# Kernel optimization log

Hardware: AMD Instinct MI355X
Metric: run time of the kernel (lower is better)

Reference implementation:

```python
import jax, jax.numpy as jnp
import numpy as np

B, S, H = 4, 4096, 1024
E, K, DE, DS = 8, 2, 128, 512  # n_routed_experts, top_k, routed hidden, shared hidden


def setup_inputs() -> dict:
    key = jax.random.key(0)
    ks = jax.random.split(key, 10)
    sc = 0.02
    return {
        "x": jax.random.normal(ks[0], (B, S, H), dtype=jnp.float32),
        "Wg": jax.random.normal(ks[1], (E, H), dtype=jnp.float32) * sc,
        "W1": jax.random.normal(ks[2], (E, DE, H), dtype=jnp.float32) * sc,
        "b1": jnp.zeros((E, DE), dtype=jnp.float32),
        "W2": jax.random.normal(ks[3], (E, H, DE), dtype=jnp.float32) * sc,
        "b2": jnp.zeros((E, H), dtype=jnp.float32),
        "Ws1": jax.random.normal(ks[4], (DS, H), dtype=jnp.float32) * sc,
        "bs1": jnp.zeros((DS,), dtype=jnp.float32),
        "Ws2": jax.random.normal(ks[5], (H, DS), dtype=jnp.float32) * sc,
        "bs2": jnp.zeros((H,), dtype=jnp.float32),
    }


def reference(x, Wg, W1, b1, W2, b2, Ws1, bs1, Ws2, bs2):
    # FFNMoE forward, eval mode (dropout = identity, aux loss inactive).
    xf = x.reshape(-1, H)  # [T, H]
    # --- MOEGate: softmax scoring + top-k + normalized weights ---
    logits = xf @ Wg.T                         # [T, E]
    scores = jax.nn.softmax(logits, axis=-1)
    topk_w, topk_idx = jax.lax.top_k(scores, K)  # [T, K]
    topk_w = topk_w / (jnp.sum(topk_w, axis=-1, keepdims=True) + 1e-20)
    # Dense per-(token, expert) combine weight (topk indices are distinct).
    w = jnp.sum(jax.nn.one_hot(topk_idx, E, dtype=xf.dtype) * topk_w[..., None], axis=1)  # [T, E]
    # --- Routed experts: fc1 -> relu -> fc2, weighted scatter-combine ---
    h1 = jax.nn.relu(jnp.einsum('th,efh->tef', xf, W1) + b1)       # [T, E, DE]
    y = jnp.einsum('tef,ehf,te->th', h1, W2, w) + w @ b2           # [T, H]
    # --- Shared expert ---
    sh = jax.nn.relu(xf @ Ws1.T + bs1) @ Ws2.T + bs2               # [T, H]
    return (y + sh).reshape(x.shape)
```

## Files before the change

### kernel.cpp

```cpp
#include <hip/hip_runtime.h>
#include <cstdint>

#define TTOK 16384
#define HD   1024
#define NE   8
#define NDE  128
#define NDS  512
#define NC1  1536
#define KC2  1536
#define NPAIR 28
#define MAXT  96
#define PREPB 3080
#define GATEB 1024
#define NH    768

typedef float  f32x4  __attribute__((ext_vector_type(4)));
typedef __bf16 bf16x8 __attribute__((ext_vector_type(8)));

__device__ __forceinline__ unsigned short f2bf(float f) {
  unsigned int u = __float_as_uint(f);
  u += 0x7fffu + ((u >> 16) & 1u);
  return (unsigned short)(u >> 16);
}

__device__ __forceinline__ void gl2lds16(const void* gp, void* lp) {
  void* g0 = const_cast<void*>(gp);
  __builtin_amdgcn_global_load_lds((__attribute__((address_space(1))) void*)g0,
                                   (__attribute__((address_space(3))) void*)lp,
                                   16, 0, 0);
}

__device__ __forceinline__ void barx() {
  asm volatile("" ::: "memory");
  __builtin_amdgcn_s_barrier();
  asm volatile("" ::: "memory");
}

template<int Q>
__device__ __forceinline__ void phase_reads(const unsigned short* Ab, const unsigned short* Bb,
                                            int bs, int a0, int b0,
                                            bf16x8 (&av)[4][2], bf16x8 (&bv)[2][2]) {
  constexpr int MH = Q >> 1, NHF = Q & 1;
  if constexpr (NHF == 0) {
#pragma unroll
    for (int m = 0; m < 4; ++m) {
      const int ao = a0 + (MH * 4 + m) * 1024;
      av[m][0] = *(const bf16x8*)(Ab + bs + ao);
      av[m][1] = *(const bf16x8*)(Ab + bs + (ao ^ 32));
    }
  }
#pragma unroll
  for (int n = 0; n < 2; ++n) {
    const int bo = b0 + (NHF * 2 + n) * 1024;
    bv[n][0] = *(const bf16x8*)(Bb + bs + bo);
    bv[n][1] = *(const bf16x8*)(Bb + bs + (bo ^ 32));
  }
}

template<int Q>
__device__ __forceinline__ void phase_mfma(bf16x8 (&av)[4][2], bf16x8 (&bv)[2][2],
                                           f32x4 (&acc)[8][4]) {
  constexpr int MH = Q >> 1, NHF = Q & 1;
  __builtin_amdgcn_s_setprio(1);
#pragma unroll
  for (int ks = 0; ks < 2; ++ks)
#pragma unroll
    for (int m = 0; m < 4; ++m)
#pragma unroll
      for (int n = 0; n < 2; ++n)
        acc[MH * 4 + m][NHF * 2 + n] = __builtin_amdgcn_mfma_f32_16x16x32_bf16(
            av[m][ks], bv[n][ks], acc[MH * 4 + m][NHF * 2 + n], 0, 0, 0);
  __builtin_amdgcn_s_setprio(0);
}

#define PH(Q, BH, STG, VMW) do {                                    \
    phase_reads<Q>(AsB, BsB, (BH) * 16384, a0, b0, av, bv);         \
    STG;                                                            \
    VMW;                                                            \
    barx();                                                         \
    asm volatile("s_waitcnt lgkmcnt(0)" ::: "memory");              \
    __builtin_amdgcn_sched_barrier(0);                              \
    phase_mfma<Q>(av, bv, acc);                                     \
    barx();                                                         \
  } while (0)

__global__ __launch_bounds__(256) void prep_gate(
    const float* __restrict__ x, const float* __restrict__ Wg,
    const float* __restrict__ W1, const float* __restrict__ Ws1,
    const float* __restrict__ W2, const float* __restrict__ Ws2,
    const float* __restrict__ b1, const float* __restrict__ bs1,
    unsigned short* __restrict__ W1cat, unsigned short* __restrict__ W2cat,
    float* __restrict__ bias1, unsigned short* __restrict__ xbf,
    float2* __restrict__ wpair, int* __restrict__ pid) {
  if (blockIdx.x < PREPB) {
    const int total = NC1 * HD + HD * KC2 + NC1;
    for (int idx = blockIdx.x * 256 + threadIdx.x; idx < total; idx += PREPB * 256) {
      if (idx < NC1 * HD) {
        int r = idx >> 10, k = idx & 1023;
        float v = (r < 1024) ? W1[idx] : Ws1[(size_t)(r - 1024) * HD + k];
        W1cat[idx] = f2bf(v);
      } else if (idx < NC1 * HD + HD * KC2) {
        int i2 = idx - NC1 * HD;
        int h = i2 / KC2;
        int j = i2 - h * KC2;
        float v = (j < 1024) ? W2[(size_t)((j >> 7) * HD + h) * NDE + (j & 127)]
                             : Ws2[(size_t)h * NDS + (j - 1024)];
        W2cat[i2] = f2bf(v);
      } else {
        int r = idx - (NC1 * HD + HD * KC2);
        bias1[r] = (r < 1024) ? b1[r] : bs1[r - 1024];
      }
    }
    return;
  }
  __shared__ float part[16 * 8 * 64];
  __shared__ float lgs[128];

  const int tid  = threadIdx.x;
  const int lane = tid & 63;
  const int wv   = tid >> 6;
  const int g    = blockIdx.x - PREPB;
  const int tokb = g * 16 + wv * 4;

  const float* xr = x + (size_t)tokb * HD + lane * 16;
  float4 xv[4][4];
#pragma unroll
  for (int t = 0; t < 4; ++t)
#pragma unroll
    for (int c = 0; c < 4; ++c)
      xv[t][c] = ((const float4*)(xr + (size_t)t * HD))[c];

#pragma unroll
  for (int t = 0; t < 4; ++t) {
    unsigned short* xo = xbf + (size_t)(tokb + t) * HD + lane * 16;
    union { unsigned short us[8]; uint4 v; } pk;
    pk.us[0] = f2bf(xv[t][0].x); pk.us[1] = f2bf(xv[t][0].y);
    pk.us[2] = f2bf(xv[t][0].z); pk.us[3] = f2bf(xv[t][0].w);
    pk.us[4] = f2bf(xv[t][1].x); pk.us[5] = f2bf(xv[t][1].y);
    pk.us[6] = f2bf(xv[t][1].z); pk.us[7] = f2bf(xv[t][1].w);
    ((uint4*)xo)[0] = pk.v;
    pk.us[0] = f2bf(xv[t][2].x); pk.us[1] = f2bf(xv[t][2].y);
    pk.us[2] = f2bf(xv[t][2].z); pk.us[3] = f2bf(xv[t][2].w);
    pk.us[4] = f2bf(xv[t][3].x); pk.us[5] = f2bf(xv[t][3].y);
    pk.us[6] = f2bf(xv[t][3].z); pk.us[7] = f2bf(xv[t][3].w);
    ((uint4*)xo)[1] = pk.v;
  }

  float p[4][8];
#pragma unroll
  for (int t = 0; t < 4; ++t)
#pragma unroll
    for (int e = 0; e < 8; ++e) p[t][e] = 0.f;
#pragma unroll
  for (int e = 0; e < 8; ++e) {
    const float4* wr = (const float4*)(Wg + (size_t)e * HD + lane * 16);
    float4 w0 = wr[0], w1 = wr[1], w2 = wr[2], w3 = wr[3];
#pragma unroll
    for (int t = 0; t < 4; ++t) {
      p[t][e] = w0.x * xv[t][0].x + w0.y * xv[t][0].y + w0.z * xv[t][0].z + w0.w * xv[t][0].w +
                w1.x * xv[t][1].x + w1.y * xv[t][1].y + w1.z * xv[t][1].z + w1.w * xv[t][1].w +
                w2.x * xv[t][2].x + w2.y * xv[t][2].y + w2.z * xv[t][2].z + w2.w * xv[t][2].w +
                w3.x * xv[t][3].x + w3.y * xv[t][3].y + w3.z * xv[t][3].z + w3.w * xv[t][3].w;
    }
  }
#pragma unroll
  for (int t = 0; t < 4; ++t)
#pragma unroll
    for (int e = 0; e < 8; ++e) {
      int j = (wv * 4 + t) * 8 + e;
      part[j * 64 + ((lane + 4 * j) & 63)] = p[t][e];
    }
  __syncthreads();

  if (tid < 128) {
    float s = 0.f;
#pragma unroll
    for (int m = 0; m < 16; ++m) {
      int kk = (4 * m + 4 * tid) & 63;
      float4 v = *(const float4*)&part[tid * 64 + kk];
      s += v.x + v.y + v.z + v.w;
    }
    lgs[tid] = s;
  }
  __syncthreads();

  if (tid < 16) {
    float lg[8];
#pragma unroll
    for (int e = 0; e < 8; ++e) lg[e] = lgs[tid * 8 + e];
    int i1 = 0; float m1 = lg[0];
#pragma unroll
    for (int e = 1; e < 8; ++e) { if (lg[e] > m1) { m1 = lg[e]; i1 = e; } }
    int i2 = -1; float m2 = -3.4e38f;
#pragma unroll
    for (int e = 0; e < 8; ++e) { if (e != i1 && lg[e] > m2) { m2 = lg[e]; i2 = e; } }
    float Z = 0.f;
#pragma unroll
    for (int e = 0; e < 8; ++e) Z += expf(lg[e] - m1);
    float s1 = 1.f / Z;
    float s2 = expf(m2 - m1) / Z;
    float dn = s1 + s2 + 1e-20f;
    float w1 = s1 / dn, w2 = s2 / dn;
    int ef, es; float wf, wsx;
    if (i1 < i2) { ef = i1; es = i2; wf = w1; wsx = w2; }
    else         { ef = i2; es = i1; wf = w2; wsx = w1; }
    int pq = ef * 7 - (ef * (ef - 1)) / 2 + (es - ef - 1);
    int t = g * 16 + tid;
    wpair[t] = make_float2(wf, wsx);
    pid[t] = pq;
  }
}

__global__ __launch_bounds__(256) void route_scan(const int* __restrict__ pid,
                                                  int* __restrict__ perm,
                                                  int4* __restrict__ tiletab,
                                                  int* __restrict__ ntct) {
  __shared__ int hist[256 * 29];
  __shared__ int totals[NPAIR];
  __shared__ int spre[256];
  const int p   = blockIdx.x;
  const int tid = threadIdx.x;
#pragma unroll
  for (int q = 0; q < 29; ++q) hist[tid * 29 + q] = 0;
  __syncthreads();
  for (int k = 0; k < 64; ++k) {
    int q = pid[tid + (k << 8)];
    hist[tid * 29 + q]++;
  }
  __syncthreads();
  if (tid < NPAIR) {
    int s = 0;
    for (int i = 0; i < 256; ++i) s += hist[i * 29 + tid];
    totals[tid] = s;
  }
  __syncthreads();
  const int mycnt = hist[tid * 29 + p];
  spre[tid] = mycnt;
  __syncthreads();
  for (int d = 1; d < 256; d <<= 1) {
    int add = (tid >= d) ? spre[tid - d] : 0;
    __syncthreads();
    spre[tid] += add;
    __syncthreads();
  }
  int estart = 0, tstart = 0;
  for (int q = 0; q < p; ++q) { estart += totals[q]; tstart += (totals[q] + 255) >> 8; }
  const int cp = totals[p];
  const int nt = (cp + 255) >> 8;
  if (p == NPAIR - 1 && tid == 0) ntct[0] = tstart + nt;
  for (int k = tid; k < nt; k += 256) {
    int4 e;
    e.x = p;
    e.y = estart + (k << 8);
    e.z = min(256, cp - (k << 8));
    e.w = (tstart + k) << 8;
    tiletab[tstart + k] = e;
  }
  int wr = estart + spre[tid] - mycnt;
  for (int k = 0; k < 64; ++k) {
    int t = tid + (k << 8);
    if (pid[t] == p) perm[wr++] = t;
  }
}

__global__ __launch_bounds__(512, 2) void moe_fc1(
    const unsigned short* __restrict__ xbf, const unsigned short* __restrict__ W1cat,
    const int* __restrict__ perm, const float2* __restrict__ wpair,
    const float* __restrict__ bias1, const int4* __restrict__ tiletab,
    const int* __restrict__ ntct, unsigned short* __restrict__ Hbuf) {
  const int L   = blockIdx.x;
  const int xcd = L & 7;
  const int s   = L >> 3;
  const int mg  = s / 3;
  const int nn  = s - mg * 3;
  const int mt  = xcd + (mg << 3);
  if (mt >= ntct[0]) return;
  const int4 tt = tiletab[mt];
  const int eoff = tt.y, valid = tt.z, hbase = tt.w;
  int ef = 0, rem = tt.x;
  while (rem >= 7 - ef) { rem -= 7 - ef; ef++; }
  const int es = ef + 1 + rem;

  __shared__ __align__(16) unsigned short As[2 * 16384];
  __shared__ __align__(16) unsigned short Bs[2 * 16384];

  const int tid  = threadIdx.x;
  const int lane = tid & 63;
  const int wv   = tid >> 6;
  const int wm   = wv >> 2;
  const int wn   = wv & 3;
  const int r16  = lane & 15;
  const int quad = lane >> 4;

  const unsigned short* gAp[2][2];
  const unsigned short* gBp[2][2];
  int lAo[2][2], lBo[2][2];
#pragma unroll
  for (int h = 0; h < 2; ++h)
#pragma unroll
    for (int jj = 0; jj < 2; ++jj) {
      const int id = jj * 512 + tid;
      const int rp = id >> 3, cc = id & 7;
      const int rowA = h * 64 + ((rp & 64) << 1) + (rp & 63);
      const int tok  = perm[eoff + min(rowA, valid - 1)];
      gAp[h][jj] = xbf + (size_t)tok * HD + ((cc ^ (rowA & 7)) << 3);
      lAo[h][jj] = rowA * 64 + cc * 8;
      const int rowB = h * 128 + rp;
      const int brow = (nn == 0) ? (((h == 0) ? ef : es) * 128 + rp)
                                 : 1024 + (nn - 1) * 256 + rowB;
      gBp[h][jj] = W1cat + (size_t)brow * HD + ((cc ^ (rowB & 7)) << 3);
      lBo[h][jj] = rowB * 64 + cc * 8;
    }

  unsigned short* AsB = As;
  unsigned short* BsB = Bs;

  const int swz = (quad ^ (r16 & 7)) << 3;
  const int a0 = (wm * 128 + r16) * 64 + swz;
  const int b0 = (wn * 64 + r16) * 64 + swz;

  f32x4 acc[8][4];
#pragma unroll
  for (int i = 0; i < 8; ++i)
#pragma unroll
    for (int j = 0; j < 4; ++j) acc[i][j] = (f32x4){0.f, 0.f, 0.f, 0.f};
  bf16x8 av[4][2], bv[2][2];

#define STG_A1K(t, h) do { const int b_ = (((t) & 1) << 14); const int o_ = ((t) << 6); \
    gl2lds16(gAp[h][0] + o_, AsB + b_ + lAo[h][0]);                                     \
    gl2lds16(gAp[h][1] + o_, AsB + b_ + lAo[h][1]); } while (0)
#define STG_B1K(t, h) do { const int b_ = (((t) & 1) << 14); const int o_ = ((t) << 6); \
    gl2lds16(gBp[h][0] + o_, BsB + b_ + lBo[h][0]);                                     \
    gl2lds16(gBp[h][1] + o_, BsB + b_ + lBo[h][1]); } while (0)

  STG_A1K(0, 0); STG_A1K(0, 1);
  STG_B1K(0, 0); STG_B1K(0, 1);
  STG_A1K(1, 0); STG_A1K(1, 1);
  asm volatile("s_waitcnt vmcnt(4)" ::: "memory");
  barx();

#define FC1_ITER(it, LASTF) do {                                                   \
    const int O1 = 2 * (it) + 1, E2 = 2 * (it) + 2, O2 = 2 * (it) + 3;             \
    PH(0, 0, STG_B1K(O1, 0), (void)0);                                             \
    PH(1, 0, STG_B1K(O1, 1), (void)0);                                             \
    PH(2, 0, { if (!(LASTF)) STG_A1K(E2, 0); }, (void)0);                          \
    PH(3, 0, { if (!(LASTF)) STG_A1K(E2, 1); },                                    \
        { if (LASTF) asm volatile("s_waitcnt vmcnt(0)" ::: "memory");              \
          else       asm volatile("s_waitcnt vmcnt(4)" ::: "memory"); });          \
    PH(0, 1, { if (!(LASTF)) STG_B1K(E2, 0); }, (void)0);                          \
    PH(1, 1, { if (!(LASTF)) STG_B1K(E2, 1); }, (void)0);                          \
    PH(2, 1, { if (!(LASTF)) STG_A1K(O2, 0); }, (void)0);                          \
    PH(3, 1, { if (!(LASTF)) STG_A1K(O2, 1); },                                    \
        { if (LASTF) asm volatile("s_waitcnt vmcnt(0)" ::: "memory");              \
          else       asm volatile("s_waitcnt vmcnt(4)" ::: "memory"); });          \
  } while (0)

#pragma unroll 1
  for (int it = 0; it < 7; ++it) FC1_ITER(it, 0);
  FC1_ITER(7, 1);

  __syncthreads();
  float2* wl = (float2*)As;
  if (tid < 256) {
    const int tokc = perm[eoff + min(tid, valid - 1)];
    wl[tid] = wpair[tokc];
  }
  __syncthreads();
  float bz[4];
  const int colb = wn * 64 + r16;
#pragma unroll
  for (int n2 = 0; n2 < 4; ++n2) {
    const int col = colb + n2 * 16;
    const int bidx = (nn == 0) ? ((col < 128) ? ef * 128 + col : es * 128 + (col - 128))
                               : 1024 + (nn - 1) * 256 + col;
    bz[n2] = bias1[bidx];
  }
#pragma unroll
  for (int m2 = 0; m2 < 8; ++m2) {
#pragma unroll
    for (int r = 0; r < 4; ++r) {
      const int lrow = wm * 128 + m2 * 16 + quad * 4 + r;
      const float2 w = wl[lrow];
      const float sc = (nn == 0) ? ((wn < 2) ? w.x : w.y) : 1.0f;
      unsigned short* hp = Hbuf + (size_t)(hbase + lrow) * NH + nn * 256 + colb;
#pragma unroll
      for (int n2 = 0; n2 < 4; ++n2) {
        const float v = fmaxf(acc[m2][n2][r] + bz[n2], 0.f) * sc;
        hp[n2 * 16] = f2bf(v);
      }
    }
  }
#undef FC1_ITER
#undef STG_A1K
#undef STG_B1K
}

__device__ __forceinline__ int koB2(int t, int ef, int es) {
  return (t < 2) ? ef * 128 + (t << 6)
       : (t < 4) ? es * 128 + ((t - 2) << 6)
                 : 1024 + ((t - 4) << 6);
}

__global__ __launch_bounds__(512, 2) void moe_fc2(
    const unsigned short* __restrict__ Hbuf, const unsigned short* __restrict__ W2cat,
    const int* __restrict__ perm, const float2* __restrict__ wpair,
    const float* __restrict__ b2, const float* __restrict__ bs2,
    const int4* __restrict__ tiletab, const int* __restrict__ ntct,
    float* __restrict__ out) {
  const int L   = blockIdx.x;
  const int xcd = L & 7;
  const int s   = L >> 3;
  const int mg  = s >> 2;
  const int nn  = s & 3;
  const int mt  = xcd + (mg << 3);
  if (mt >= ntct[0]) return;
  const int4 tt = tiletab[mt];
  const int eoff = tt.y, valid = tt.z, hbase = tt.w;
  int ef = 0, rem = tt.x;
  while (rem >= 7 - ef) { rem -= 7 - ef; ef++; }
  const int es = ef + 1 + rem;
  const int tileN = nn << 8;

  __shared__ __align__(16) unsigned short As[2 * 16384];
  __shared__ __align__(16) unsigned short Bs[2 * 16384];

  const int tid  = threadIdx.x;
  const int lane = tid & 63;
  const int wv   = tid >> 6;
  const int wm   = wv >> 2;
  const int wn   = wv & 3;
  const int r16  = lane & 15;
  const int quad = lane >> 4;

  const unsigned short* gAp[2][2];
  const unsigned short* gBp[2][2];
  int lAo[2][2], lBo[2][2];
#pragma unroll
  for (int h = 0; h < 2; ++h)
#pragma unroll
    for (int jj = 0; jj < 2; ++jj) {
      const int id = jj * 512 + tid;
      const int rp = id >> 3, cc = id & 7;
      const int rowA = h * 64 + ((rp & 64) << 1) + (rp & 63);
      gAp[h][jj] = Hbuf + (size_t)(hbase + rowA) * NH + ((cc ^ (rowA & 7)) << 3);
      lAo[h][jj] = rowA * 64 + cc * 8;
      const int rowB = h * 128 + rp;
      gBp[h][jj] = W2cat + (size_t)(tileN + rowB) * KC2 + ((cc ^ (rowB & 7)) << 3);
      lBo[h][jj] = rowB * 64 + cc * 8;
    }

  unsigned short* AsB = As;
  unsigned short* BsB = Bs;

  const int swz = (quad ^ (r16 & 7)) << 3;
  const int a0 = (wm * 128 + r16) * 64 + swz;
  const int b0 = (wn * 64 + r16) * 64 + swz;

  f32x4 acc[8][4];
#pragma unroll
  for (int i = 0; i < 8; ++i)
#pragma unroll
    for (int j = 0; j < 4; ++j) acc[i][j] = (f32x4){0.f, 0.f, 0.f, 0.f};
  bf16x8 av[4][2], bv[2][2];

#define STG_A2K(t, h) do { const int b_ = (((t) & 1) << 14); const int o_ = ((t) << 6); \
    gl2lds16(gAp[h][0] + o_, AsB + b_ + lAo[h][0]);                                     \
    gl2lds16(gAp[h][1] + o_, AsB + b_ + lAo[h][1]); } while (0)
#define STG_B2K(t, h) do { const int b_ = (((t) & 1) << 14); const int o_ = koB2((t), ef, es); \
    gl2lds16(gBp[h][0] + o_, BsB + b_ + lBo[h][0]);                                     \
    gl2lds16(gBp[h][1] + o_, BsB + b_ + lBo[h][1]); } while (0)

  STG_A2K(0, 0); STG_A2K(0, 1);
  STG_B2K(0, 0); STG_B2K(0, 1);
  STG_A2K(1, 0); STG_A2K(1, 1);
  asm volatile("s_waitcnt vmcnt(4)" ::: "memory");
  barx();

#define FC2_ITER(it, LASTF) do {                                                   \
    const int O1 = 2 * (it) + 1, E2 = 2 * (it) + 2, O2 = 2 * (it) + 3;             \
    PH(0, 0, STG_B2K(O1, 0), (void)0);                                             \
    PH(1, 0, STG_B2K(O1, 1), (void)0);                                             \
    PH(2, 0, { if (!(LASTF)) STG_A2K(E2, 0); }, (void)0);                          \
    PH(3, 0, { if (!(LASTF)) STG_A2K(E2, 1); },                                    \
        { if (LASTF) asm volatile("s_waitcnt vmcnt(0)" ::: "memory");              \
          else       asm volatile("s_waitcnt vmcnt(4)" ::: "memory"); });          \
    PH(0, 1, { if (!(LASTF)) STG_B2K(E2, 0); }, (void)0);                          \
    PH(1, 1, { if (!(LASTF)) STG_B2K(E2, 1); }, (void)0);                          \
    PH(2, 1, { if (!(LASTF)) STG_A2K(O2, 0); }, (void)0);                          \
    PH(3, 1, { if (!(LASTF)) STG_A2K(O2, 1); },                                    \
        { if (LASTF) asm volatile("s_waitcnt vmcnt(0)" ::: "memory");              \
          else       asm volatile("s_waitcnt vmcnt(4)" ::: "memory"); });          \
  } while (0)

#pragma unroll 1
  for (int it = 0; it < 5; ++it) FC2_ITER(it, 0);
  FC2_ITER(5, 1);

  __syncthreads();
  float2* wl2 = (float2*)As;
  int* tokl   = (int*)Bs;
  if (tid < 256) {
    const int tokc = perm[eoff + min(tid, valid - 1)];
    tokl[tid] = (tid < valid) ? tokc : -1;
    wl2[tid] = wpair[tokc];
  }
  __syncthreads();
  float bsc[4], b2a[4], b2b[4];
  const int colb = tileN + wn * 64 + r16;
#pragma unroll
  for (int n2 = 0; n2 < 4; ++n2) {
    const int col = colb + n2 * 16;
    bsc[n2] = bs2[col];
    b2a[n2] = b2[(size_t)ef * HD + col];
    b2b[n2] = b2[(size_t)es * HD + col];
  }
#pragma unroll
  for (int m2 = 0; m2 < 8; ++m2) {
#pragma unroll
    for (int r = 0; r < 4; ++r) {
      const int lrow = wm * 128 + m2 * 16 + quad * 4 + r;
      const int tok = tokl[lrow];
      if (tok < 0) continue;
      const float2 w = wl2[lrow];
      float* op = out + (size_t)tok * HD + colb;
#pragma unroll
      for (int n2 = 0; n2 < 4; ++n2)
        op[n2 * 16] = acc[m2][n2][r] + bsc[n2] + w.x * b2a[n2] + w.y * b2b[n2];
    }
  }
#undef FC2_ITER
#undef STG_A2K
#undef STG_B2K
}

extern "C" void kernel_launch(void* const* d_in, const int* in_sizes, int n_in,
                              void* d_out, int out_size, void* d_ws, size_t ws_size,
                              hipStream_t stream) {
  const float* x   = (const float*)d_in[0];
  const float* Wg  = (const float*)d_in[1];
  const float* W1  = (const float*)d_in[2];
  const float* b1  = (const float*)d_in[3];
  const float* W2  = (const float*)d_in[4];
  const float* b2  = (const float*)d_in[5];
  const float* Ws1 = (const float*)d_in[6];
  const float* bs1 = (const float*)d_in[7];
  const float* Ws2 = (const float*)d_in[8];
  const float* bs2 = (const float*)d_in[9];

  char* ws = (char*)d_ws;
  size_t off = 0;
  unsigned short* xbf   = (unsigned short*)(ws + off); off += (size_t)TTOK * HD * 2;
  unsigned short* Hbuf  = (unsigned short*)(ws + off); off += (size_t)MAXT * 256 * NH * 2;
  unsigned short* W1cat = (unsigned short*)(ws + off); off += (size_t)NC1 * HD * 2;
  unsigned short* W2cat = (unsigned short*)(ws + off); off += (size_t)HD * KC2 * 2;
  float* bias1          = (float*)(ws + off);          off += (size_t)NC1 * 4;
  float2* wpair         = (float2*)(ws + off);         off += (size_t)TTOK * 8;
  int* pid              = (int*)(ws + off);            off += (size_t)TTOK * 4;
  int* perm             = (int*)(ws + off);            off += (size_t)TTOK * 4;
  int4* tiletab         = (int4*)(ws + off);           off += (size_t)MAXT * 16;
  int* ntct             = (int*)(ws + off);            off += 16;

  prep_gate<<<PREPB + GATEB, 256, 0, stream>>>(x, Wg, W1, Ws1, W2, Ws2, b1, bs1,
                                               W1cat, W2cat, bias1, xbf, wpair, pid);
  route_scan<<<NPAIR, 256, 0, stream>>>(pid, perm, tiletab, ntct);
  moe_fc1<<<8 * 12 * 3, 512, 0, stream>>>(xbf, W1cat, perm, wpair, bias1, tiletab, ntct, Hbuf);
  moe_fc2<<<8 * 12 * 4, 512, 0, stream>>>(Hbuf, W2cat, perm, wpair, b2, bs2, tiletab, ntct,
                                          (float*)d_out);
}
```

Before: 294.7 us.

## Reschedule fc1 staging pipeline and replace fc2 with smaller-tile single-buffered GEMM

The fc1 kernel's global-to-LDS staging schedule is reshuffled: A half-tiles are issued earlier, vmcnt waits are tightened to 2, partial lgkmcnt waits are added, and the sched_barrier is dropped. The fc2 kernel is replaced by a simpler 128x128-tile, 256-thread kernel with a single LDS buffer and 16 blocks per routing tile. This adds occupancy and parallelism for fc2 but gives up its double-buffered phased pipeline, so load latency is exposed at each of the two syncthreads per K step. Fewer accumulators per thread also lowers register pressure.

```diff
diff --git a/kernel.cpp b/kernel.cpp
--- a/kernel.cpp
+++ b/kernel.cpp
@@ -58,8 +58,8 @@
 }
 
 template<int Q>
-__device__ __forceinline__ void phase_mfma(bf16x8 (&av)[4][2], bf16x8 (&bv)[2][2],
-                                           f32x4 (&acc)[8][4]) {
+__device__ __forceinline__ void phase_mfma2(bf16x8 (&av)[4][2], bf16x8 (&bv)[2][2],
+                                            f32x4 (&acc)[8][4]) {
   constexpr int MH = Q >> 1, NHF = Q & 1;
   __builtin_amdgcn_s_setprio(1);
 #pragma unroll
@@ -73,16 +73,20 @@
   __builtin_amdgcn_s_setprio(0);
 }
 
-#define PH(Q, BH, STG, VMW) do {                                    \
+#define PH(Q, BH, STG, VMW, PRELG) do {                             \
     phase_reads<Q>(AsB, BsB, (BH) * 16384, a0, b0, av, bv);         \
     STG;                                                            \
     VMW;                                                            \
+    PRELG;                                                          \
     barx();                                                         \
     asm volatile("s_waitcnt lgkmcnt(0)" ::: "memory");              \
-    __builtin_amdgcn_sched_barrier(0);                              \
-    phase_mfma<Q>(av, bv, acc);                                     \
+    phase_mfma2<Q>(av, bv, acc);                                    \
     barx();                                                         \
   } while (0)
+
+#define LG8  asm volatile("s_waitcnt lgkmcnt(8)" ::: "memory")
+#define VM2  asm volatile("s_waitcnt vmcnt(2)" ::: "memory")
+#define VM0  asm volatile("s_waitcnt vmcnt(0)" ::: "memory")
 
 __global__ __launch_bounds__(256) void prep_gate(
     const float* __restrict__ x, const float* __restrict__ Wg,
@@ -335,24 +339,20 @@
 
   STG_A1K(0, 0); STG_A1K(0, 1);
   STG_B1K(0, 0); STG_B1K(0, 1);
-  STG_A1K(1, 0); STG_A1K(1, 1);
-  asm volatile("s_waitcnt vmcnt(4)" ::: "memory");
+  STG_A1K(1, 0);
+  VM2;
   barx();
 
-#define FC1_ITER(it, LASTF) do {                                                   \
-    const int O1 = 2 * (it) + 1, E2 = 2 * (it) + 2, O2 = 2 * (it) + 3;             \
-    PH(0, 0, STG_B1K(O1, 0), (void)0);                                             \
-    PH(1, 0, STG_B1K(O1, 1), (void)0);                                             \
-    PH(2, 0, { if (!(LASTF)) STG_A1K(E2, 0); }, (void)0);                          \
-    PH(3, 0, { if (!(LASTF)) STG_A1K(E2, 1); },                                    \
-        { if (LASTF) asm volatile("s_waitcnt vmcnt(0)" ::: "memory");              \
-          else       asm volatile("s_waitcnt vmcnt(4)" ::: "memory"); });          \
-    PH(0, 1, { if (!(LASTF)) STG_B1K(E2, 0); }, (void)0);                          \
-    PH(1, 1, { if (!(LASTF)) STG_B1K(E2, 1); }, (void)0);                          \
-    PH(2, 1, { if (!(LASTF)) STG_A1K(O2, 0); }, (void)0);                          \
-    PH(3, 1, { if (!(LASTF)) STG_A1K(O2, 1); },                                    \
-        { if (LASTF) asm volatile("s_waitcnt vmcnt(0)" ::: "memory");              \
-          else       asm volatile("s_waitcnt vmcnt(4)" ::: "memory"); });          \
+#define FC1_ITER(it, LASTF) do {                                                    \
+    const int T1 = 2 * (it) + 1, T2 = 2 * (it) + 2, T3 = 2 * (it) + 3;              \
+    PH(0, 0, { STG_A1K(T1, 1); STG_B1K(T1, 0); }, (void)0, LG8);                    \
+    PH(1, 0, { STG_B1K(T1, 1); }, (void)0, (void)0);                                \
+    PH(2, 0, { if (!(LASTF)) STG_A1K(T2, 0); }, (void)0, LG8);                      \
+    PH(3, 0, (void)0, { if (LASTF) { VM0; } else { VM2; } }, (void)0);              \
+    PH(0, 1, { if (!(LASTF)) { STG_A1K(T2, 1); STG_B1K(T2, 0); } }, (void)0, LG8);  \
+    PH(1, 1, { if (!(LASTF)) STG_B1K(T2, 1); }, (void)0, (void)0);                  \
+    PH(2, 1, { if (!(LASTF)) STG_A1K(T3, 0); }, (void)0, LG8);                      \
+    PH(3, 1, (void)0, { if (!(LASTF)) { VM2; } }, (void)0);                         \
   } while (0)
 
 #pragma unroll 1
@@ -395,142 +395,135 @@
 #undef STG_B1K
 }
 
-__device__ __forceinline__ int koB2(int t, int ef, int es) {
-  return (t < 2) ? ef * 128 + (t << 6)
-       : (t < 4) ? es * 128 + ((t - 2) << 6)
-                 : 1024 + ((t - 4) << 6);
-}
-
-__global__ __launch_bounds__(512, 2) void moe_fc2(
-    const unsigned short* __restrict__ Hbuf, const unsigned short* __restrict__ W2cat,
-    const int* __restrict__ perm, const float2* __restrict__ wpair,
-    const float* __restrict__ b2, const float* __restrict__ bs2,
-    const int4* __restrict__ tiletab, const int* __restrict__ ntct,
-    float* __restrict__ out) {
+__global__ __launch_bounds__(256) void moe_fc2(const unsigned short* __restrict__ Hbuf,
+                                               const unsigned short* __restrict__ W2cat,
+                                               const int* __restrict__ perm,
+                                               const float2* __restrict__ wpair,
+                                               const float* __restrict__ b2,
+                                               const float* __restrict__ bs2,
+                                               const int4* __restrict__ tiletab,
+                                               const int* __restrict__ ntct,
+                                               float* __restrict__ out) {
   const int L   = blockIdx.x;
   const int xcd = L & 7;
   const int s   = L >> 3;
-  const int mg  = s >> 2;
-  const int nn  = s & 3;
+  const int mg  = s >> 4;
+  const int rm  = s & 15;
+  const int mh  = rm >> 3;
+  const int nn  = rm & 7;
   const int mt  = xcd + (mg << 3);
   if (mt >= ntct[0]) return;
   const int4 tt = tiletab[mt];
-  const int eoff = tt.y, valid = tt.z, hbase = tt.w;
+  const int v128 = tt.z - (mh << 7);
+  if (v128 <= 0) return;
+  const int eoff = tt.y + (mh << 7);
+  const int valid = min(128, v128);
+  const int hbase = tt.w + (mh << 7);
   int ef = 0, rem = tt.x;
   while (rem >= 7 - ef) { rem -= 7 - ef; ef++; }
   const int es = ef + 1 + rem;
-  const int tileN = nn << 8;
-
-  __shared__ __align__(16) unsigned short As[2 * 16384];
-  __shared__ __align__(16) unsigned short Bs[2 * 16384];
+  const int tileN = nn << 7;
+
+  __shared__ __align__(16) unsigned short As[128 * 64];
+  __shared__ __align__(16) unsigned short Bs[128 * 64];
 
   const int tid  = threadIdx.x;
   const int lane = tid & 63;
   const int wv   = tid >> 6;
-  const int wm   = wv >> 2;
-  const int wn   = wv & 3;
+  const int wm   = wv >> 1;
+  const int wn   = wv & 1;
   const int r16  = lane & 15;
   const int quad = lane >> 4;
 
-  const unsigned short* gAp[2][2];
-  const unsigned short* gBp[2][2];
-  int lAo[2][2], lBo[2][2];
-#pragma unroll
-  for (int h = 0; h < 2; ++h)
-#pragma unroll
-    for (int jj = 0; jj < 2; ++jj) {
-      const int id = jj * 512 + tid;
-      const int rp = id >> 3, cc = id & 7;
-      const int rowA = h * 64 + ((rp & 64) << 1) + (rp & 63);
-      gAp[h][jj] = Hbuf + (size_t)(hbase + rowA) * NH + ((cc ^ (rowA & 7)) << 3);
-      lAo[h][jj] = rowA * 64 + cc * 8;
-      const int rowB = h * 128 + rp;
-      gBp[h][jj] = W2cat + (size_t)(tileN + rowB) * KC2 + ((cc ^ (rowB & 7)) << 3);
-      lBo[h][jj] = rowB * 64 + cc * 8;
-    }
-
-  unsigned short* AsB = As;
-  unsigned short* BsB = Bs;
-
-  const int swz = (quad ^ (r16 & 7)) << 3;
-  const int a0 = (wm * 128 + r16) * 64 + swz;
-  const int b0 = (wn * 64 + r16) * 64 + swz;
-
-  f32x4 acc[8][4];
-#pragma unroll
-  for (int i = 0; i < 8; ++i)
+  const unsigned short* gA[4];
+  const unsigned short* gB[4];
+  unsigned short* lA[4];
+  unsigned short* lB[4];
+#pragma unroll
+  for (int i = 0; i < 4; ++i) {
+    int idx = i * 256 + tid;
+    int row = idx >> 3;
+    int cc  = idx & 7;
+    int kc  = cc ^ (row & 7);
+    gA[i] = Hbuf + (size_t)(hbase + row) * NH + kc * 8;
+    gB[i] = W2cat + (size_t)(tileN + row) * KC2 + kc * 8;
+    lA[i] = As + idx * 8;
+    lB[i] = Bs + idx * 8;
+  }
+
+  int aoff[4], boff[4];
+#pragma unroll
+  for (int i = 0; i < 4; ++i) {
+    int ra = wm * 64 + i * 16 + r16;
+    aoff[i] = ra * 64 + ((quad ^ (ra & 7)) << 3);
+    int rb = wn * 64 + i * 16 + r16;
+    boff[i] = rb * 64 + ((quad ^ (rb & 7)) << 3);
+  }
+
+  f32x4 acc[4][4];
+#pragma unroll
+  for (int i = 0; i < 4; ++i)
 #pragma unroll
     for (int j = 0; j < 4; ++j) acc[i][j] = (f32x4){0.f, 0.f, 0.f, 0.f};
-  bf16x8 av[4][2], bv[2][2];
-
-#define STG_A2K(t, h) do { const int b_ = (((t) & 1) << 14); const int o_ = ((t) << 6); \
-    gl2lds16(gAp[h][0] + o_, AsB + b_ + lAo[h][0]);                                     \
-    gl2lds16(gAp[h][1] + o_, AsB + b_ + lAo[h][1]); } while (0)
-#define STG_B2K(t, h) do { const int b_ = (((t) & 1) << 14); const int o_ = koB2((t), ef, es); \
-    gl2lds16(gBp[h][0] + o_, BsB + b_ + lBo[h][0]);                                     \
-    gl2lds16(gBp[h][1] + o_, BsB + b_ + lBo[h][1]); } while (0)
-
-  STG_A2K(0, 0); STG_A2K(0, 1);
-  STG_B2K(0, 0); STG_B2K(0, 1);
-  STG_A2K(1, 0); STG_A2K(1, 1);
-  asm volatile("s_waitcnt vmcnt(4)" ::: "memory");
-  barx();
-
-#define FC2_ITER(it, LASTF) do {                                                   \
-    const int O1 = 2 * (it) + 1, E2 = 2 * (it) + 2, O2 = 2 * (it) + 3;             \
-    PH(0, 0, STG_B2K(O1, 0), (void)0);                                             \
-    PH(1, 0, STG_B2K(O1, 1), (void)0);                                             \
-    PH(2, 0, { if (!(LASTF)) STG_A2K(E2, 0); }, (void)0);                          \
-    PH(3, 0, { if (!(LASTF)) STG_A2K(E2, 1); },                                    \
-        { if (LASTF) asm volatile("s_waitcnt vmcnt(0)" ::: "memory");              \
-          else       asm volatile("s_waitcnt vmcnt(4)" ::: "memory"); });          \
-    PH(0, 1, { if (!(LASTF)) STG_B2K(E2, 0); }, (void)0);                          \
-    PH(1, 1, { if (!(LASTF)) STG_B2K(E2, 1); }, (void)0);                          \
-    PH(2, 1, { if (!(LASTF)) STG_A2K(O2, 0); }, (void)0);                          \
-    PH(3, 1, { if (!(LASTF)) STG_A2K(O2, 1); },                                    \
-        { if (LASTF) asm volatile("s_waitcnt vmcnt(0)" ::: "memory");              \
-          else       asm volatile("s_waitcnt vmcnt(4)" ::: "memory"); });          \
-  } while (0)
-
-#pragma unroll 1
-  for (int it = 0; it < 5; ++it) FC2_ITER(it, 0);
-  FC2_ITER(5, 1);
-
-  __syncthreads();
+
+  for (int kt = 0; kt < 12; ++kt) {
+    const int koA = kt << 6;
+    const int koB = (kt < 2) ? ef * 128 + (kt << 6)
+                 : (kt < 4) ? es * 128 + ((kt - 2) << 6)
+                            : 1024 + ((kt - 4) << 6);
+#pragma unroll
+    for (int i = 0; i < 4; ++i) gl2lds16(gA[i] + koA, lA[i]);
+#pragma unroll
+    for (int i = 0; i < 4; ++i) gl2lds16(gB[i] + koB, lB[i]);
+    __syncthreads();
+#pragma unroll
+    for (int g = 0; g < 2; ++g) {
+      const int gx = g << 5;
+      bf16x8 av[4], bvv[4];
+#pragma unroll
+      for (int i = 0; i < 4; ++i) av[i] = *(const bf16x8*)(As + (aoff[i] ^ gx));
+#pragma unroll
+      for (int j = 0; j < 4; ++j) bvv[j] = *(const bf16x8*)(Bs + (boff[j] ^ gx));
+#pragma unroll
+      for (int i = 0; i < 4; ++i)
+#pragma unroll
+        for (int j = 0; j < 4; ++j)
+          acc[i][j] = __builtin_amdgcn_mfma_f32_16x16x32_bf16(av[i], bvv[j], acc[i][j], 0, 0, 0);
+    }
+    __syncthreads();
+  }
+
   float2* wl2 = (float2*)As;
   int* tokl   = (int*)Bs;
-  if (tid < 256) {
-    const int tokc = perm[eoff + min(tid, valid - 1)];
+  if (tid < 128) {
+    int tokc = perm[eoff + min(tid, valid - 1)];
     tokl[tid] = (tid < valid) ? tokc : -1;
     wl2[tid] = wpair[tokc];
   }
   __syncthreads();
   float bsc[4], b2a[4], b2b[4];
-  const int colb = tileN + wn * 64 + r16;
-#pragma unroll
-  for (int n2 = 0; n2 < 4; ++n2) {
-    const int col = colb + n2 * 16;
-    bsc[n2] = bs2[col];
-    b2a[n2] = b2[(size_t)ef * HD + col];
-    b2b[n2] = b2[(size_t)es * HD + col];
-  }
-#pragma unroll
-  for (int m2 = 0; m2 < 8; ++m2) {
+#pragma unroll
+  for (int j = 0; j < 4; ++j) {
+    const int col = tileN + wn * 64 + j * 16 + r16;
+    bsc[j] = bs2[col];
+    b2a[j] = b2[(size_t)ef * HD + col];
+    b2b[j] = b2[(size_t)es * HD + col];
+  }
+#pragma unroll
+  for (int i = 0; i < 4; ++i) {
 #pragma unroll
     for (int r = 0; r < 4; ++r) {
-      const int lrow = wm * 128 + m2 * 16 + quad * 4 + r;
+      const int lrow = wm * 64 + i * 16 + quad * 4 + r;
       const int tok = tokl[lrow];
       if (tok < 0) continue;
       const float2 w = wl2[lrow];
-      float* op = out + (size_t)tok * HD + colb;
-#pragma unroll
-      for (int n2 = 0; n2 < 4; ++n2)
-        op[n2 * 16] = acc[m2][n2][r] + bsc[n2] + w.x * b2a[n2] + w.y * b2b[n2];
-    }
-  }
-#undef FC2_ITER
-#undef STG_A2K
-#undef STG_B2K
+#pragma unroll
+      for (int j = 0; j < 4; ++j) {
+        const int col = tileN + wn * 64 + j * 16 + r16;
+        out[(size_t)tok * HD + col] = acc[i][j][r] + bsc[j] + w.x * b2a[j] + w.y * b2b[j];
+      }
+    }
+  }
 }
 
 extern "C" void kernel_launch(void* const* d_in, const int* in_sizes, int n_in,
@@ -564,6 +557,6 @@
                                                W1cat, W2cat, bias1, xbf, wpair, pid);
   route_scan<<<NPAIR, 256, 0, stream>>>(pid, perm, tiletab, ntct);
   moe_fc1<<<8 * 12 * 3, 512, 0, stream>>>(xbf, W1cat, perm, wpair, bias1, tiletab, ntct, Hbuf);
-  moe_fc2<<<8 * 12 * 4, 512, 0, stream>>>(Hbuf, W2cat, perm, wpair, b2, bs2, tiletab, ntct,
-                                          (float*)d_out);
-}
+  moe_fc2<<<8 * 12 * 16, 256, 0, stream>>>(Hbuf, W2cat, perm, wpair, b2, bs2, tiletab, ntct,
+                                           (float*)d_out);
+}
```

After: 279.7 us. 1.05x faster.
